# Optimization experiments

Measured on AMD Instinct MI355X. Metric: run time of the kernel, lower is better.

The kernel has to match this reference:

```python
import jax, jax.numpy as jnp
import numpy as np

C = 128          # num_channels
HID = 256        # mlp hidden = 2*C
HEAD_DIM = 16    # C // num_heads (8)
SCALE = 1.0 / np.sqrt(HEAD_DIM)
EPS = 1e-5


def _linear_init(key, fan_in, fan_out):
    kw, kb = jax.random.split(key)
    s = 1.0 / np.sqrt(fan_in)
    w = jax.random.uniform(kw, (fan_in, fan_out), minval=-s, maxval=s, dtype=jnp.float32)
    b = jax.random.uniform(kb, (fan_out,), minval=-s, maxval=s, dtype=jnp.float32)
    return w, b


def setup_inputs() -> dict:
    key = jax.random.key(0)
    ks = jax.random.split(key, 8)
    x = jax.random.normal(ks[0], (4, C, 64, 64), dtype=jnp.float32)
    wq, bq = _linear_init(ks[1], C, C)
    wk, bk = _linear_init(ks[2], C, C)
    wv, bv = _linear_init(ks[3], C, C)
    wo, bo = _linear_init(ks[4], C, C)
    w1, b1 = _linear_init(ks[5], C, HID)
    w2, b2 = _linear_init(ks[6], HID, C)
    return {
        "x": x,
        "ln1_w": jnp.ones((C,), jnp.float32), "ln1_b": jnp.zeros((C,), jnp.float32),
        "wq": wq, "bq": bq, "wk": wk, "bk": bk, "wv": wv, "bv": bv,
        "wo": wo, "bo": bo,
        "ln2_w": jnp.ones((C,), jnp.float32), "ln2_b": jnp.zeros((C,), jnp.float32),
        "w1": w1, "b1": b1, "w2": w2, "b2": b2,
    }


def _layernorm(x, w, b):
    mu = jnp.mean(x, axis=-1, keepdims=True)
    var = jnp.mean(jnp.square(x - mu), axis=-1, keepdims=True)
    return (x - mu) * jax.lax.rsqrt(var + EPS) * w + b


def reference(x, ln1_w, ln1_b, wq, bq, wk, bk, wv, bv, wo, bo, ln2_w, ln2_b, w1, b1, w2, b2):
    B, Cc, H, W = x.shape
    t = x.reshape(B, Cc, H * W).transpose(0, 2, 1)  # [B, S, C]
    xl = _layernorm(t, ln1_w, ln1_b)
    q = xl @ wq + bq
    k = xl @ wk + bk
    v = xl @ wv + bv
    scores = jnp.einsum('bqc,bkc->bqk', q, k) * SCALE  # [B, S, S]
    # Faithful to source: softmax over dim=1 (the QUERY axis).
    attn = jax.nn.softmax(scores, axis=1)
    att_out = jnp.einsum('bqk,bkc->bqc', attn, v) @ wo + bo
    t = att_out + t
    m = _layernorm(t, ln2_w, ln2_b) @ w1 + b1
    m = jax.nn.gelu(m, approximate=False) @ w2 + b2
    t = jax.nn.gelu(m, approximate=False) + t  # second GELU per source
    return t.transpose(0, 2, 1).reshape(B, Cc, H, W)
```

## Files before the change

kernel.cpp:

```cpp
#include <hip/hip_runtime.h>
#include <math.h>

#define S 4096
#define CNUM 128
#define BATCH 4
#define MTOT (BATCH * S)
#define SCLOG2E 0.36067376022224085f
#define EPSLN 1e-5f
#define KSPLIT 8
#define QSPLIT 8


typedef __attribute__((ext_vector_type(8))) short bf16x8;
typedef __attribute__((ext_vector_type(4))) float f32x4;
typedef __attribute__((ext_vector_type(16))) float f32x16;
typedef __attribute__((ext_vector_type(4))) unsigned int u32x4;

__device__ __forceinline__ float gelu_exact(float x) {
    return 0.5f * x * (1.0f + erff(x * 0.7071067811865476f));
}

__device__ __forceinline__ unsigned short f2b(float f) {
    union { float f; unsigned int u; } v; v.f = f;
    unsigned int r = (v.u + 0x7FFFu + ((v.u >> 16) & 1u)) >> 16;
    return (unsigned short)r;
}
__device__ __forceinline__ float b2f(unsigned short u) {
    return __uint_as_float((unsigned)u << 16);
}
__device__ __forceinline__ int swz(int col, int row) {
    return ((((col >> 3) ^ (row & 15)) << 3) | (col & 7));
}

__device__ __forceinline__ void gl_lds16(const void* g, void* l) {
    __builtin_amdgcn_global_load_lds(
        (__attribute__((address_space(1))) void*)g,
        (__attribute__((address_space(3))) void*)l, 16, 0, 0);
}

__global__ __launch_bounds__(256) void ln1_transpose(
    const float* __restrict__ x, const float* __restrict__ w, const float* __restrict__ bb,
    unsigned short* __restrict__ xlh, float* __restrict__ t)
{
    __shared__ float tile[128][65];
    __shared__ float mu[64], rs[64];
    const int b = blockIdx.y;
    const int s0 = blockIdx.x * 64;
    const float* xb = x + (size_t)b * CNUM * S;
    for (int i = threadIdx.x; i < 128 * 64; i += 256) {
        int c = i >> 6, sl = i & 63;
        tile[c][sl] = xb[(size_t)c * S + s0 + sl];
    }
    __syncthreads();
    if (threadIdx.x < 64) {
        float sum = 0.f, sq = 0.f;
        for (int c = 0; c < 128; ++c) {
            float v = tile[c][threadIdx.x];
            sum += v; sq += v * v;
        }
        float m = sum * (1.f / 128.f);
        float var = sq * (1.f / 128.f) - m * m;
        mu[threadIdx.x] = m;
        rs[threadIdx.x] = rsqrtf(var + EPSLN);
    }
    __syncthreads();
    for (int i = threadIdx.x; i < 128 * 64; i += 256) {
        int c = i & 127, sl = i >> 7;
        float v = tile[c][sl];
        size_t row = (size_t)b * S + s0 + sl;
        t[row * CNUM + c] = v;
        xlh[row * CNUM + swz(c, sl)] = f2b((v - mu[sl]) * rs[sl] * w[c] + bb[c]);
    }
}

__global__ __launch_bounds__(256) void convw(
    const float* __restrict__ wq, const float* __restrict__ wk, const float* __restrict__ wv,
    const float* __restrict__ wo, const float* __restrict__ w1, const float* __restrict__ w2,
    const float* __restrict__ bq, const float* __restrict__ bk, const float* __restrict__ bv,
    unsigned short* __restrict__ wqkvh, unsigned short* __restrict__ woh,
    unsigned short* __restrict__ w1h, unsigned short* __restrict__ w2h,
    float* __restrict__ bqkv)
{
    int a = blockIdx.y;
    int idx = blockIdx.x * 256 + threadIdx.x;
    if (a == 6) {
        if (idx < 128) bqkv[idx] = bq[idx];
        else if (idx < 256) bqkv[idx] = bk[idx - 128];
        else if (idx < 384) bqkv[idx] = bv[idx - 256];
        return;
    }
    const float* src; unsigned short* dst; int Nsh, Ksz;
    switch (a) {
        case 0: src = wq; dst = wqkvh;          Nsh = 7; Ksz = 128; break;
        case 1: src = wk; dst = wqkvh + 16384;  Nsh = 7; Ksz = 128; break;
        case 2: src = wv; dst = wqkvh + 32768;  Nsh = 7; Ksz = 128; break;
        case 3: src = wo; dst = woh;            Nsh = 7; Ksz = 128; break;
        case 4: src = w1; dst = w1h;            Nsh = 8; Ksz = 128; break;
        default: src = w2; dst = w2h;           Nsh = 7; Ksz = 256; break;
    }
    int total = Ksz << Nsh;
    if (idx >= total) return;
    int k = idx >> Nsh, n = idx & ((1 << Nsh) - 1);
    dst[n * Ksz + swz(k, n)] = f2b(src[idx]);
}

template<int KT, int EPI, int BM>
__global__ __launch_bounds__(256) void gemm_mfma(
    const unsigned short* __restrict__ A, const unsigned short* __restrict__ Bt,
    const float* __restrict__ bias, const float* __restrict__ res,
    void* __restrict__ Cv, void* __restrict__ Cv2,
    const float* __restrict__ wln, const float* __restrict__ bln, int N)
{
    constexpr int CH = KT / 8;
    constexpr int CSH = (KT == 128) ? 4 : 5;
    constexpr int BKT = (KT == 256) ? 128 : KT;
    constexpr int NPH = KT / BKT;
    constexpr int NJ = (BM == 64) ? 4 : 2;
    constexpr int NG = 128 / (NJ * 16);
    __shared__ unsigned short As[BM * KT];
    __shared__ unsigned short Bs[128 * BKT];
    __shared__ float2 lnred[(EPI == 3) ? NG * BM : 1];
    const int bm = blockIdx.y * BM;
    const int bn = blockIdx.x * 128;
    const int z = blockIdx.z;
    const unsigned short* Btz = (EPI == 7) ? Bt + z * 16384 : Bt;
    const float* biasz = (EPI == 7) ? bias + z * 128 : bias;
    const int tid = threadIdx.x;
    const int w = tid >> 6, l = tid & 63;
    const int rw = (BM == 64) ? (w & 1) * 32 : 0;
    const int cw = (BM == 64) ? (w >> 1) * 64 : w * 32;
    const int lm = l & 15, lq = l >> 4;

    f32x4 zero = {0.f, 0.f, 0.f, 0.f};
    f32x4 acc[2][NJ];
    #pragma unroll
    for (int i = 0; i < 2; ++i)
        #pragma unroll
        for (int j = 0; j < NJ; ++j) acc[i][j] = zero;

    #pragma unroll
    for (int ph = 0; ph < NPH; ++ph) {
        if (ph == 0) {
            if (EPI == 3) {
                #pragma unroll
                for (int i = 0; i < (BM * CH) / 256; ++i) {
                    int cid = i * 256 + tid;
                    int r = cid >> CSH, c = cid & (CH - 1);
                    int p = (c & ~15) | ((c ^ r) & 15);
                    float s8[8];
                    #pragma unroll
                    for (int j = 0; j < 8; ++j) s8[j] = 0.f;
                    #pragma unroll
                    for (int pp = 0; pp < KSPLIT; ++pp) {
                        const unsigned short* src = A + (size_t)pp * ((size_t)MTOT * CNUM)
                                                      + (size_t)(bm + r) * KT + c * 8;
                        ushort4 u0 = *(const ushort4*)(src);
                        ushort4 u1 = *(const ushort4*)(src + 4);
                        s8[0] += b2f(u0.x); s8[1] += b2f(u0.y); s8[2] += b2f(u0.z); s8[3] += b2f(u0.w);
                        s8[4] += b2f(u1.x); s8[5] += b2f(u1.y); s8[6] += b2f(u1.z); s8[7] += b2f(u1.w);
                    }
                    ushort4 o0, o1;
                    o0.x = f2b(s8[0]); o0.y = f2b(s8[1]); o0.z = f2b(s8[2]); o0.w = f2b(s8[3]);
                    o1.x = f2b(s8[4]); o1.y = f2b(s8[5]); o1.z = f2b(s8[6]); o1.w = f2b(s8[7]);
                    *(ushort4*)(As + r * KT + p * 8) = o0;
                    *(ushort4*)(As + r * KT + p * 8 + 4) = o1;
                }
            } else {
                #pragma unroll
                for (int i = 0; i < (BM * CH) / 256; ++i)
                    gl_lds16(A + (size_t)bm * KT + (i * 256 + tid) * 8,
                             As + (i * 256 + tid) * 8);
            }
        } else {
            __syncthreads();
        }
        #pragma unroll
        for (int i = 0; i < (128 * BKT / 8) / 256; ++i) {
            int cid = i * 256 + tid;
            int n = cid >> (CSH - (NPH - 1)), gg = cid & (BKT / 8 - 1);
            gl_lds16(Btz + (size_t)(bn + n) * KT + ph * BKT + gg * 8,
                     Bs + cid * 8);
        }
        __syncthreads();

        #pragma unroll
        for (int ks = 0; ks < BKT / 32; ++ks) {
            int c_loc = ks * 4 + lq;
            int c_glob = ph * 16 + c_loc;
            bf16x8 a[2], bfr[NJ];
            #pragma unroll
            for (int i = 0; i < 2; ++i) {
                int m = rw + i * 16 + lm;
                int p = (c_glob & ~15) | ((c_glob ^ m) & 15);
                a[i] = *(const bf16x8*)(As + m * KT + p * 8);
            }
            #pragma unroll
            for (int j = 0; j < NJ; ++j) {
                int n = cw + j * 16 + lm;
                int p = (c_loc ^ n) & 15;
                bfr[j] = *(const bf16x8*)(Bs + n * BKT + p * 8);
            }
            #pragma unroll
            for (int i = 0; i < 2; ++i)
                #pragma unroll
                for (int j = 0; j < NJ; ++j)
                    acc[i][j] = __builtin_amdgcn_mfma_f32_16x16x32_bf16(a[i], bfr[j], acc[i][j], 0, 0, 0);
        }
    }

    if (EPI == 3) {
        float vv[2][NJ][4];
        #pragma unroll
        for (int i = 0; i < 2; ++i) {
            int rowbase = bm + rw + i * 16 + lq * 4;
            #pragma unroll
            for (int j = 0; j < NJ; ++j) {
                int col = bn + cw + j * 16 + lm;
                #pragma unroll
                for (int reg = 0; reg < 4; ++reg)
                    vv[i][j][reg] = acc[i][j][reg] + biasz[col] +
                                    res[(size_t)(rowbase + reg) * N + col];
            }
        }
        #pragma unroll
        for (int i = 0; i < 2; ++i)
            #pragma unroll
            for (int reg = 0; reg < 4; ++reg) {
                float s = 0.f, q = 0.f;
                #pragma unroll
                for (int j = 0; j < NJ; ++j) {
                    float xv = vv[i][j][reg];
                    s += xv; q += xv * xv;
                }
                #pragma unroll
                for (int off = 1; off < 16; off <<= 1) {
                    s += __shfl_xor(s, off);
                    q += __shfl_xor(q, off);
                }
                if (lm == 0) {
                    float2 sq2; sq2.x = s; sq2.y = q;
                    lnred[(cw / (NJ * 16)) * BM + rw + i * 16 + lq * 4 + reg] = sq2;
                }
            }
        __syncthreads();
        #pragma unroll
        for (int i = 0; i < 2; ++i) {
            #pragma unroll
            for (int reg = 0; reg < 4; ++reg) {
                int lrow = rw + i * 16 + lq * 4 + reg;
                int row = bm + lrow;
                float sx = 0.f, sq = 0.f;
                #pragma unroll
                for (int g = 0; g < NG; ++g) {
                    float2 h = lnred[g * BM + lrow];
                    sx += h.x; sq += h.y;
                }
                float mean = sx * (1.f / 128.f);
                float var  = sq * (1.f / 128.f) - mean * mean;
                float rs = rsqrtf(var + EPSLN);
                #pragma unroll
                for (int j = 0; j < NJ; ++j) {
                    int col = bn + cw + j * 16 + lm;
                    float xv = vv[i][j][reg];
                    ((float*)Cv)[(size_t)row * N + col] = xv;
                    ((unsigned short*)Cv2)[(size_t)row * N + swz(col, lrow)] =
                        f2b((xv - mean) * rs * wln[col] + bln[col]);
                }
            }
        }
        return;
    }

    #pragma unroll
    for (int i = 0; i < 2; ++i) {
        int rowbase = bm + rw + i * 16 + lq * 4;
        #pragma unroll
        for (int j = 0; j < NJ; ++j) {
            int col = bn + cw + j * 16 + lm;
            float v[4];
            #pragma unroll
            for (int reg = 0; reg < 4; ++reg) v[reg] = acc[i][j][reg] + biasz[col];
            if (EPI == 6) {
                #pragma unroll
                for (int reg = 0; reg < 4; ++reg)
                    ((unsigned short*)Cv)[(size_t)(rowbase + reg) * N + swz(col, rowbase + reg)] =
                        f2b(gelu_exact(v[reg]));
            } else if (EPI == 8) {
                int bb = rowbase >> 12, s = rowbase & 4095;
                float4 o;
                o.x = gelu_exact(v[0]) + res[(size_t)(rowbase + 0) * N + col];
                o.y = gelu_exact(v[1]) + res[(size_t)(rowbase + 1) * N + col];
                o.z = gelu_exact(v[2]) + res[(size_t)(rowbase + 2) * N + col];
                o.w = gelu_exact(v[3]) + res[(size_t)(rowbase + 3) * N + col];
                *(float4*)(((float*)Cv) + ((size_t)(bb * 128 + col)) * 4096 + s) = o;
            } else if (EPI == 7) {
                if (z < 2) {
                    unsigned short* dst = ((unsigned short*)Cv) + (size_t)z * MTOT * 128;
                    #pragma unroll
                    for (int reg = 0; reg < 4; ++reg) {
                        float ov = (z == 0) ? v[reg] * SCLOG2E : v[reg];
                        dst[(size_t)(rowbase + reg) * 128 + swz(col, rowbase + reg)] = f2b(ov);
                    }
                } else {
                    int bb = rowbase >> 12, s = rowbase & 4095;
                    int kc = s >> 6, g = (s >> 3) & 7;
                    ushort4 o;
                    o.x = f2b(v[0]); o.y = f2b(v[1]); o.z = f2b(v[2]); o.w = f2b(v[3]);
                    *(ushort4*)(((unsigned short*)Cv) + (size_t)2 * MTOT * 128 +
                                (((size_t)bb * 64 + kc) << 13) +
                                col * 64 + ((g ^ (col & 7)) << 3) + (s & 7)) = o;
                }
            }
        }
    }
}

__global__ __launch_bounds__(256) void colsum(
    const unsigned short* __restrict__ qh, const unsigned short* __restrict__ kh,
    float* __restrict__ psum_all)
{
    __shared__ unsigned short Qs[128 * 128];
    __shared__ unsigned short Ks[128 * 128];
    __shared__ float csum[2][128];
    const int b = blockIdx.z;
    const unsigned short* Q = qh + (size_t)b * S * 128;
    const unsigned short* Km = kh + (size_t)b * S * 128;
    const int bn = blockIdx.x * 128;
    const int q0 = blockIdx.y * (S / QSPLIT);
    const int tid = threadIdx.x;
    const int w = tid >> 6, l = tid & 63;
    const int wr = (w >> 1) * 64, wc = (w & 1) * 64;
    const int lm = l & 15, lq = l >> 4;

    #pragma unroll
    for (int i = 0; i < 8; ++i)
        gl_lds16(Km + (size_t)bn * 128 + (i * 256 + tid) * 8, Ks + (i * 256 + tid) * 8);

    float jsum[4] = {0.f, 0.f, 0.f, 0.f};
    for (int qt = 0; qt < (S / QSPLIT) / 128; ++qt) {
        __syncthreads();
        #pragma unroll
        for (int i = 0; i < 8; ++i)
            gl_lds16(Q + (size_t)(q0 + qt * 128) * 128 + (i * 256 + tid) * 8,
                     Qs + (i * 256 + tid) * 8);
        __syncthreads();

        f32x4 zero = {0.f, 0.f, 0.f, 0.f};
        f32x4 acc[4][4];
        #pragma unroll
        for (int i = 0; i < 4; ++i)
            #pragma unroll
            for (int j = 0; j < 4; ++j) acc[i][j] = zero;

        #pragma unroll
        for (int ks = 0; ks < 4; ++ks) {
            bf16x8 a[4], bfr[4];
            #pragma unroll
            for (int i = 0; i < 4; ++i) {
                int m = wr + i * 16 + lm;
                int p = (ks * 4 + lq) ^ (m & 15);
                a[i] = *(const bf16x8*)(Qs + m * 128 + p * 8);
            }
            #pragma unroll
            for (int j = 0; j < 4; ++j) {
                int n = wc + j * 16 + lm;
                int p = (ks * 4 + lq) ^ (n & 15);
                bfr[j] = *(const bf16x8*)(Ks + n * 128 + p * 8);
            }
            #pragma unroll
            for (int i = 0; i < 4; ++i)
                #pragma unroll
                for (int j = 0; j < 4; ++j)
                    acc[i][j] = __builtin_amdgcn_mfma_f32_16x16x32_bf16(a[i], bfr[j], acc[i][j], 0, 0, 0);
        }

        #pragma unroll
        for (int i = 0; i < 4; ++i)
            #pragma unroll
            for (int j = 0; j < 4; ++j)
                #pragma unroll
                for (int reg = 0; reg < 4; ++reg)
                    jsum[j] += exp2f(acc[i][j][reg]);
    }

    #pragma unroll
    for (int j = 0; j < 4; ++j) {
        jsum[j] += __shfl_xor(jsum[j], 16);
        jsum[j] += __shfl_xor(jsum[j], 32);
    }
    if (l < 16) {
        #pragma unroll
        for (int j = 0; j < 4; ++j)
            csum[w >> 1][wc + j * 16 + l] = jsum[j];
    }
    __syncthreads();
    if (tid < 128)
        psum_all[((size_t)(blockIdx.y * BATCH + b)) * S + bn + tid] = csum[0][tid] + csum[1][tid];
}

__global__ __launch_bounds__(256) void vscale(
    unsigned short* __restrict__ Vimg_all, const float* __restrict__ psum_all)
{
    const int b = blockIdx.z;
    unsigned short* Vimg = Vimg_all + (size_t)b * CNUM * S;
    int i = (blockIdx.x * 256 + threadIdx.x) * 4;
    int kc = i >> 13;
    int off = i & 8191;
    int c = off >> 6;
    int p = (off >> 3) & 7;
    int g = p ^ (c & 7);
    int k = kc * 64 + g * 8 + (off & 7);
    float4 L = *(const float4*)(psum_all + (size_t)b * S + k);
    #pragma unroll
    for (int t = 1; t < QSPLIT; ++t) {
        float4 Lt = *(const float4*)(psum_all + ((size_t)(t * BATCH + b)) * S + k);
        L.x += Lt.x; L.y += Lt.y; L.z += Lt.z; L.w += Lt.w;
    }
    ushort4 v = *(ushort4*)(Vimg + i);
    v.x = f2b(b2f(v.x) / L.x);
    v.y = f2b(b2f(v.y) / L.y);
    v.z = f2b(b2f(v.z) / L.z);
    v.w = f2b(b2f(v.w) / L.w);
    *(ushort4*)(Vimg + i) = v;
}

__global__ __launch_bounds__(256, 2) void fused_attnv(
    const unsigned short* __restrict__ qh, const unsigned short* __restrict__ kh,
    const unsigned short* __restrict__ Vimg_all, unsigned short* __restrict__ parts)
{
    __shared__ unsigned short Ks[32 * 128];
    __shared__ unsigned short Vls[128 * 64];
    const int b = blockIdx.z;
    const unsigned short* Qm = qh + (size_t)b * S * 128;
    const unsigned short* Km = kh + (size_t)b * S * 128;
    const unsigned short* Vimg = Vimg_all + (((size_t)b * 64) << 13);
    unsigned short* Pout = parts + (size_t)blockIdx.x * ((size_t)MTOT * CNUM)
                                 + (size_t)b * S * CNUM;
    const int q0 = blockIdx.y * 128;
    const int kb0 = blockIdx.x * (S / KSPLIT);
    const int kc0 = blockIdx.x * (S / KSPLIT / 64);
    const int tid = threadIdx.x;
    const int w = tid >> 6, l = tid & 63;
    const int lc = l & 31, lh = l >> 5;
    const int row0 = q0 + w * 32;

    bf16x8 aq[8];
    #pragma unroll
    for (int d = 0; d < 8; ++d)
        aq[d] = *(const bf16x8*)(Qm + (size_t)(row0 + lc) * 128 +
                                 (((d * 2 + lh) ^ (lc & 15)) << 3));

    f32x16 acco[4];
    #pragma unroll
    for (int cb = 0; cb < 4; ++cb)
        #pragma unroll
        for (int r = 0; r < 16; ++r) acco[cb][r] = 0.f;

    for (int kt = 0; kt < S / KSPLIT / 32; ++kt) {
        const int kb = kb0 + kt * 32;
        if (kt) __syncthreads();
        #pragma unroll
        for (int i2 = 0; i2 < 2; ++i2)
            gl_lds16(Km + (size_t)kb * 128 + (i2 * 256 + tid) * 8,
                     Ks + (i2 * 256 + tid) * 8);
        if ((kt & 1) == 0) {
            const unsigned short* src = Vimg + ((size_t)(kc0 + (kt >> 1)) << 13) + tid * 8;
            #pragma unroll
            for (int i2 = 0; i2 < 4; ++i2)
                gl_lds16(src + i2 * 2048, &Vls[(i2 * 256 + tid) * 8]);
        }
        __syncthreads();

        f32x16 accT;
        #pragma unroll
        for (int r = 0; r < 16; ++r) accT[r] = 0.f;
        #pragma unroll
        for (int d = 0; d < 8; ++d) {
            int slot = d * 2 + lh;
            bf16x8 kf = *(const bf16x8*)(Ks + lc * 128 + ((slot ^ (lc & 15)) << 3));
            accT = __builtin_amdgcn_mfma_f32_32x32x16_bf16(kf, aq[d], accT, 0, 0, 0);
        }

        unsigned int pk[4][2];
        #pragma unroll
        for (int t = 0; t < 4; ++t)
            #pragma unroll
            for (int p = 0; p < 2; ++p) {
                float e0 = exp2f(accT[t * 4 + 2 * p]);
                float e1 = exp2f(accT[t * 4 + 2 * p + 1]);
                asm("v_cvt_pk_bf16_f32 %0, %1, %2" : "=v"(pk[t][p]) : "v"(e0), "v"(e1));
            }
        #pragma unroll
        for (int p = 0; p < 2; ++p) {
            asm volatile("v_permlane32_swap_b32 %0, %1" : "+v"(pk[0][p]), "+v"(pk[1][p]));
            asm volatile("v_permlane32_swap_b32 %0, %1" : "+v"(pk[2][p]), "+v"(pk[3][p]));
        }
        u32x4 u0 = {pk[0][0], pk[0][1], pk[1][0], pk[1][1]};
        u32x4 u1 = {pk[2][0], pk[2][1], pk[3][0], pk[3][1]};
        bf16x8 ap0 = __builtin_bit_cast(bf16x8, u0);
        bf16x8 ap1 = __builtin_bit_cast(bf16x8, u1);

        const int g0 = (kt & 1) * 4 + lh;
        const int g1 = g0 + 2;
        __builtin_amdgcn_s_setprio(1);
        #pragma unroll
        for (int cb = 0; cb < 4; ++cb) {
            int c = cb * 32 + lc;
            bf16x8 v0 = *(const bf16x8*)(Vls + c * 64 + ((g0 ^ (c & 7)) << 3));
            bf16x8 v1 = *(const bf16x8*)(Vls + c * 64 + ((g1 ^ (c & 7)) << 3));
            acco[cb] = __builtin_amdgcn_mfma_f32_32x32x16_bf16(ap0, v0, acco[cb], 0, 0, 0);
            acco[cb] = __builtin_amdgcn_mfma_f32_32x32x16_bf16(ap1, v1, acco[cb], 0, 0, 0);
        }
        __builtin_amdgcn_s_setprio(0);
    }

    #pragma unroll
    for (int cb = 0; cb < 4; ++cb)
        #pragma unroll
        for (int r = 0; r < 16; ++r) {
            int q = (r & 3) + 8 * (r >> 2) + 4 * lh;
            Pout[(size_t)(row0 + q) * CNUM + cb * 32 + lc] = f2b(acco[cb][r]);
        }
}

extern "C" void kernel_launch(void* const* d_in, const int* in_sizes, int n_in,
                              void* d_out, int out_size, void* d_ws, size_t ws_size,
                              hipStream_t stream)
{
    (void)in_sizes; (void)n_in; (void)out_size; (void)ws_size;
    const float* x    = (const float*)d_in[0];
    const float* ln1w = (const float*)d_in[1];
    const float* ln1b = (const float*)d_in[2];
    const float* wq   = (const float*)d_in[3];
    const float* bq   = (const float*)d_in[4];
    const float* wk   = (const float*)d_in[5];
    const float* bk   = (const float*)d_in[6];
    const float* wv   = (const float*)d_in[7];
    const float* bv   = (const float*)d_in[8];
    const float* wo   = (const float*)d_in[9];
    const float* bo   = (const float*)d_in[10];
    const float* ln2w = (const float*)d_in[11];
    const float* ln2b = (const float*)d_in[12];
    const float* w1   = (const float*)d_in[13];
    const float* b1   = (const float*)d_in[14];
    const float* w2   = (const float*)d_in[15];
    const float* b2   = (const float*)d_in[16];
    float* out = (float*)d_out;

    float* ws = (float*)d_ws;
    const size_t NSC = (size_t)MTOT * CNUM;
    float* t      = ws;
    float* y      = t + NSC;
    float* psum   = y + NSC;
    unsigned short* parts = (unsigned short*)(psum + (size_t)QSPLIT * BATCH * S);
    unsigned short* xlh = parts + (size_t)KSPLIT * NSC;
    unsigned short* qh  = xlh + NSC;
    unsigned short* kh  = qh + NSC;
    unsigned short* Vt  = kh + NSC;
    unsigned short* zh  = Vt + NSC;
    unsigned short* hh  = zh + NSC;
    unsigned short* wqkvh = hh + (size_t)MTOT * 256;
    unsigned short* woh = wqkvh + 3 * 16384;
    unsigned short* w1h = woh + 16384;
    unsigned short* w2h = w1h + 32768;
    float* bqkv = (float*)(w2h + 32768);

    ln1_transpose<<<dim3(S / 64, BATCH), 256, 0, stream>>>(x, ln1w, ln1b, xlh, t);
    convw<<<dim3(128, 7), 256, 0, stream>>>(wq, wk, wv, wo, w1, w2, bq, bk, bv,
                                            wqkvh, woh, w1h, w2h, bqkv);

    gemm_mfma<128, 7, 32><<<dim3(1, MTOT / 32, 3), 256, 0, stream>>>(
        xlh, wqkvh, bqkv, nullptr, qh, nullptr, nullptr, nullptr, 128);

    colsum<<<dim3(S / 128, QSPLIT, BATCH), 256, 0, stream>>>(qh, kh, psum);
    vscale<<<dim3(CNUM * S / 4 / 256, 1, BATCH), 256, 0, stream>>>(Vt, psum);
    fused_attnv<<<dim3(KSPLIT, S / 128, BATCH), 256, 0, stream>>>(qh, kh, Vt, parts);

    gemm_mfma<128, 3, 32><<<dim3(1, MTOT / 32), 256, 0, stream>>>(
        parts, woh, bo, t, y, zh, ln2w, ln2b, 128);
    gemm_mfma<128, 6, 32><<<dim3(2, MTOT / 32), 256, 0, stream>>>(
        zh, w1h, b1, nullptr, hh, nullptr, nullptr, nullptr, 256);
    gemm_mfma<256, 8, 32><<<dim3(1, MTOT / 32), 256, 0, stream>>>(
        hh, w2h, b2, y, out, nullptr, nullptr, nullptr, 128);
}
```

Measured before the change: 224.0 us.

## Double-buffer K/V tiles in fused_attnv and read Q directly in colsum

fused_attnv now uses two LDS buffers each for K and V and issues the async global-to-LDS load of the next tile before computing the current one, so one barrier per iteration replaces two. This lets memory latency overlap with the MFMA work. colsum stops staging Q in shared memory and loads the swizzled Q fragments straight from global memory, which removes the per-tile barriers and the Q LDS buffer. The trade-off is more uncoalesced global reads in colsum and higher LDS use in fused_attnv, which could reduce occupancy.

```diff
diff --git a/kernel.cpp b/kernel.cpp
--- a/kernel.cpp
+++ b/kernel.cpp
@@ -319,7 +319,6 @@
     const unsigned short* __restrict__ qh, const unsigned short* __restrict__ kh,
     float* __restrict__ psum_all)
 {
-    __shared__ unsigned short Qs[128 * 128];
     __shared__ unsigned short Ks[128 * 128];
     __shared__ float csum[2][128];
     const int b = blockIdx.z;
@@ -335,16 +334,10 @@
     #pragma unroll
     for (int i = 0; i < 8; ++i)
         gl_lds16(Km + (size_t)bn * 128 + (i * 256 + tid) * 8, Ks + (i * 256 + tid) * 8);
+    __syncthreads();
 
     float jsum[4] = {0.f, 0.f, 0.f, 0.f};
     for (int qt = 0; qt < (S / QSPLIT) / 128; ++qt) {
-        __syncthreads();
-        #pragma unroll
-        for (int i = 0; i < 8; ++i)
-            gl_lds16(Q + (size_t)(q0 + qt * 128) * 128 + (i * 256 + tid) * 8,
-                     Qs + (i * 256 + tid) * 8);
-        __syncthreads();
-
         f32x4 zero = {0.f, 0.f, 0.f, 0.f};
         f32x4 acc[4][4];
         #pragma unroll
@@ -358,8 +351,8 @@
             #pragma unroll
             for (int i = 0; i < 4; ++i) {
                 int m = wr + i * 16 + lm;
-                int p = (ks * 4 + lq) ^ (m & 15);
-                a[i] = *(const bf16x8*)(Qs + m * 128 + p * 8);
+                a[i] = *(const bf16x8*)(Q + (size_t)(q0 + qt * 128 + m) * 128 +
+                                        (((ks * 4 + lq) ^ lm) << 3));
             }
             #pragma unroll
             for (int j = 0; j < 4; ++j) {
@@ -428,8 +421,8 @@
     const unsigned short* __restrict__ qh, const unsigned short* __restrict__ kh,
     const unsigned short* __restrict__ Vimg_all, unsigned short* __restrict__ parts)
 {
-    __shared__ unsigned short Ks[32 * 128];
-    __shared__ unsigned short Vls[128 * 64];
+    __shared__ unsigned short Ks[2][32 * 128];
+    __shared__ unsigned short Vls[2][128 * 64];
     const int b = blockIdx.z;
     const unsigned short* Qm = qh + (size_t)b * S * 128;
     const unsigned short* Km = kh + (size_t)b * S * 128;
@@ -456,20 +449,35 @@
         #pragma unroll
         for (int r = 0; r < 16; ++r) acco[cb][r] = 0.f;
 
-    for (int kt = 0; kt < S / KSPLIT / 32; ++kt) {
-        const int kb = kb0 + kt * 32;
-        if (kt) __syncthreads();
-        #pragma unroll
-        for (int i2 = 0; i2 < 2; ++i2)
-            gl_lds16(Km + (size_t)kb * 128 + (i2 * 256 + tid) * 8,
-                     Ks + (i2 * 256 + tid) * 8);
-        if ((kt & 1) == 0) {
-            const unsigned short* src = Vimg + ((size_t)(kc0 + (kt >> 1)) << 13) + tid * 8;
+    {
+        const unsigned short* ksrc = Km + (size_t)kb0 * 128 + tid * 8;
+        gl_lds16(ksrc,        &Ks[0][tid * 8]);
+        gl_lds16(ksrc + 2048, &Ks[0][(256 + tid) * 8]);
+        const unsigned short* vsrc = Vimg + ((size_t)kc0 << 13) + tid * 8;
+        #pragma unroll
+        for (int i2 = 0; i2 < 4; ++i2)
+            gl_lds16(vsrc + i2 * 2048, &Vls[0][(i2 * 256 + tid) * 8]);
+    }
+    __syncthreads();
+
+    for (int kt = 0; kt < 16; ++kt) {
+        if (kt < 15) {
+            const unsigned short* ksrc = Km + (size_t)(kb0 + (kt + 1) * 32) * 128 + tid * 8;
+            unsigned short* kdst = Ks[(kt + 1) & 1];
+            gl_lds16(ksrc,        kdst + tid * 8);
+            gl_lds16(ksrc + 2048, kdst + (256 + tid) * 8);
+        }
+        if ((kt & 1) == 1 && (kt >> 1) + 1 < 8) {
+            int vn = (kt >> 1) + 1;
+            const unsigned short* vsrc = Vimg + ((size_t)(kc0 + vn) << 13) + tid * 8;
+            unsigned short* vdst = Vls[vn & 1];
             #pragma unroll
             for (int i2 = 0; i2 < 4; ++i2)
-                gl_lds16(src + i2 * 2048, &Vls[(i2 * 256 + tid) * 8]);
-        }
-        __syncthreads();
+                gl_lds16(vsrc + i2 * 2048, vdst + (i2 * 256 + tid) * 8);
+        }
+
+        const unsigned short* Kbuf = Ks[kt & 1];
+        const unsigned short* Vbuf = Vls[(kt >> 1) & 1];
 
         f32x16 accT;
         #pragma unroll
@@ -477,7 +485,7 @@
         #pragma unroll
         for (int d = 0; d < 8; ++d) {
             int slot = d * 2 + lh;
-            bf16x8 kf = *(const bf16x8*)(Ks + lc * 128 + ((slot ^ (lc & 15)) << 3));
+            bf16x8 kf = *(const bf16x8*)(Kbuf + lc * 128 + ((slot ^ (lc & 15)) << 3));
             accT = __builtin_amdgcn_mfma_f32_32x32x16_bf16(kf, aq[d], accT, 0, 0, 0);
         }
 
@@ -506,12 +514,14 @@
         #pragma unroll
         for (int cb = 0; cb < 4; ++cb) {
             int c = cb * 32 + lc;
-            bf16x8 v0 = *(const bf16x8*)(Vls + c * 64 + ((g0 ^ (c & 7)) << 3));
-            bf16x8 v1 = *(const bf16x8*)(Vls + c * 64 + ((g1 ^ (c & 7)) << 3));
+            bf16x8 v0 = *(const bf16x8*)(Vbuf + c * 64 + ((g0 ^ (c & 7)) << 3));
+            bf16x8 v1 = *(const bf16x8*)(Vbuf + c * 64 + ((g1 ^ (c & 7)) << 3));
             acco[cb] = __builtin_amdgcn_mfma_f32_32x32x16_bf16(ap0, v0, acco[cb], 0, 0, 0);
             acco[cb] = __builtin_amdgcn_mfma_f32_32x32x16_bf16(ap1, v1, acco[cb], 0, 0, 0);
         }
         __builtin_amdgcn_s_setprio(0);
+
+        if (kt < 15) __syncthreads();
     }
 
     #pragma unroll
```

After: 208.8 us. -6.8%, faster.
